# Kernel tuning notes

Measured on AMD Instinct MI355X. Metric: run time of the kernel, lower is better.

Reference implementation:

```python
import jax, jax.numpy as jnp
import numpy as np

FEA, DK, H = 512, 64, 8
B, L = 4, 2048
EPS = 1e-5


def _layernorm(x, g, b):
    mu = jnp.mean(x, axis=-1, keepdims=True)
    var = jnp.mean(jnp.square(x - mu), axis=-1, keepdims=True)
    return (x - mu) * jax.lax.rsqrt(var + EPS) * g + b


def setup_inputs() -> dict:
    key = jax.random.key(0)
    ks = jax.random.split(key, 12)
    d = {
        'qx': jax.random.normal(ks[0], (B, L, FEA), jnp.float32),
        'kx': jax.random.normal(ks[1], (B, L, FEA), jnp.float32),
        'vx': jax.random.normal(ks[2], (B, L, FEA), jnp.float32),
        'maskPAD': jax.random.randint(ks[3], (B, L, L), 0, 2, jnp.int32),
        # attention projections (stored as [in, out]); biases zero-init as in module
        'wq': jax.random.normal(ks[4], (FEA, DK * H), jnp.float32) * 0.02,
        'bq': jnp.zeros((DK * H,), jnp.float32),
        'wk': jax.random.normal(ks[5], (FEA, DK * H), jnp.float32) * 0.02,
        'bk': jnp.zeros((DK * H,), jnp.float32),
        'wv': jax.random.normal(ks[6], (FEA, DK * H), jnp.float32) * 0.02,
        'bv': jnp.zeros((DK * H,), jnp.float32),
        'wo': jax.random.normal(ks[7], (DK * H, FEA), jnp.float32) * 0.02,
        'bo': jnp.zeros((FEA,), jnp.float32),
        # FFN
        'w1': jax.random.normal(ks[8], (FEA, 4 * FEA), jnp.float32) * 0.02,
        'b1': jnp.zeros((4 * FEA,), jnp.float32),
        'w2': jax.random.normal(ks[9], (4 * FEA, FEA), jnp.float32) * 0.02,
        'b2': jnp.zeros((FEA,), jnp.float32),
        # layer norms
        'ln1_g': jnp.ones((FEA,), jnp.float32),
        'ln1_b': jnp.zeros((FEA,), jnp.float32),
        'ln2_g': jnp.ones((FEA,), jnp.float32),
        'ln2_b': jnp.zeros((FEA,), jnp.float32),
    }
    return d


def reference(qx, kx, vx, maskPAD, wq, bq, wk, bk, wv, bv, wo, bo,
              w1, b1, w2, b2, ln1_g, ln1_b, ln2_g, ln2_b):
    b, l, _ = qx.shape
    # project and split heads: [B, H, L, DK]
    q = (qx @ wq + bq).reshape(b, l, H, DK).transpose(0, 2, 1, 3)
    k = (kx @ wk + bk).reshape(b, l, H, DK).transpose(0, 2, 1, 3)
    v = (vx @ wv + bv).reshape(b, l, H, DK).transpose(0, 2, 1, 3)
    scores = jnp.einsum('bhqd,bhkd->bhqk', q, k) / np.sqrt(DK)  # [B,H,L,L]
    mask = (maskPAD == 0)[:, None, :, :]
    scores = jnp.where(mask, jnp.float32(-2 ** 15 + 1), scores)
    alpha = jax.nn.softmax(scores, axis=-1)
    z = jnp.einsum('bhqk,bhkd->bhqd', alpha, v)  # [B,H,L,DK]
    z = z.transpose(0, 2, 1, 3).reshape(b, l, H * DK)
    z = z @ wo + bo
    # post-LN FFN block (dropout = identity at inference)
    zn = _layernorm(vx + z, ln1_g, ln1_b)
    ffn = jax.nn.gelu(zn @ w1 + b1, approximate=False) @ w2 + b2
    return _layernorm(zn + ffn, ln2_g, ln2_b)
```

## Files before the change

### kernel.cpp

```cpp
#include <hip/hip_runtime.h>
#include <cstdint>


typedef __bf16 bf16;
typedef __bf16 bf16x8 __attribute__((ext_vector_type(8)));
typedef __bf16 bf16x4 __attribute__((ext_vector_type(4)));
typedef float floatx4 __attribute__((ext_vector_type(4)));

__device__ __forceinline__ floatx4 mfma_bf16(bf16x8 a, bf16x8 b, floatx4 c) {
  return __builtin_amdgcn_mfma_f32_16x16x32_bf16(a, b, c, 0, 0, 0);
}

__device__ __forceinline__ void load_lds_16(const void* g, void* l) {
  auto gp = reinterpret_cast<const void __attribute__((address_space(1)))*>(
      reinterpret_cast<uintptr_t>(g));
  auto lp = reinterpret_cast<void __attribute__((address_space(3)))*>(
      (unsigned int)reinterpret_cast<uintptr_t>(l));
  __builtin_amdgcn_global_load_lds(gp, lp, 16, 0, 0);
}

__device__ __forceinline__ float gelu_f(float x) {
  float t = 0.7978845608f * (x + 0.044715f * x * x * x);
  float e = __builtin_amdgcn_exp2f(t * 2.885390082f);
  float th = 1.0f - 2.0f * __builtin_amdgcn_rcpf(e + 1.0f);
  return 0.5f * x * (1.0f + th);
}

#define PLANE128 2064
#define PLANE64 1040
#define PSTR 72

__global__ void __launch_bounds__(256) transpose4_k(const float* __restrict__ w0,
                                                    const float* __restrict__ w1,
                                                    const float* __restrict__ w2,
                                                    const float* __restrict__ w3,
                                                    bf16* __restrict__ o0,
                                                    bf16* __restrict__ o1,
                                                    bf16* __restrict__ o2,
                                                    bf16* __restrict__ o3) {
  const float* in = (blockIdx.z == 0) ? w0 : (blockIdx.z == 1) ? w1
                    : (blockIdx.z == 2) ? w2 : w3;
  bf16* out = (blockIdx.z == 0) ? o0 : (blockIdx.z == 1) ? o1
              : (blockIdx.z == 2) ? o2 : o3;
  __shared__ float tile[32][33];
  int m0 = blockIdx.x * 32, k0 = blockIdx.y * 32;
  int tx = threadIdx.x, ty = threadIdx.y;
  for (int i = ty; i < 32; i += 8)
    tile[i][tx] = in[(size_t)(k0 + i) * 512 + m0 + tx];
  __syncthreads();
  for (int i = ty; i < 32; i += 8)
    out[(size_t)(m0 + i) * 512 + k0 + tx] = (bf16)tile[tx][i];
}

__global__ void __launch_bounds__(256) transpose_k(const float* __restrict__ in,
                                                   bf16* __restrict__ out,
                                                   int K, int M) {
  __shared__ float tile[32][33];
  int m0 = blockIdx.x * 32, k0 = blockIdx.y * 32;
  int tx = threadIdx.x, ty = threadIdx.y;
  for (int i = ty; i < 32; i += 8)
    tile[i][tx] = in[(size_t)(k0 + i) * M + m0 + tx];
  __syncthreads();
  for (int i = ty; i < 32; i += 8)
    out[(size_t)(m0 + i) * K + k0 + tx] = (bf16)tile[tx][i];
}

__global__ void __launch_bounds__(256) maskbits_k(const int* __restrict__ m,
                                                  unsigned long long* __restrict__ out) {
  int w = blockIdx.x * 4 + (threadIdx.x >> 6);
  int lane = threadIdx.x & 63;
  int v = m[(size_t)w * 64 + lane];
  unsigned long long b = __ballot(v != 0);
  if (lane == 0) out[w] = b;
}

template <int EPI>
__device__ __forceinline__ void epi_store(void* Cout, int n, int m, int M,
                                          float val) {
  if constexpr (EPI == 1) {
    int bb = n >> 11, l = n & 2047, hh = m >> 6, d = m & 63;
    ((bf16*)Cout)[((size_t)((bb * 8 + hh) * 2048 + l)) * 64 + d] = (bf16)val;
  } else if constexpr (EPI == 2) {
    int bb = n >> 11, l = n & 2047, hh = m >> 6, d = m & 63;
    ((bf16*)Cout)[((size_t)((bb * 8 + hh) * 64 + d)) * 2048 + l] = (bf16)val;
  } else if constexpr (EPI == 3) {
    ((bf16*)Cout)[(size_t)n * M + m] = (bf16)gelu_f(val);
  } else if constexpr (EPI == 4) {
    ((float*)Cout)[(size_t)n * M + m] = val;
  } else {
    ((float*)Cout)[(size_t)n * M + m] += val;
  }
}

template <int EPI, bool TALL>
__global__ void __launch_bounds__(256) gemm_bt(const bf16* __restrict__ A,
                                               const bf16* __restrict__ Bt,
                                               const float* __restrict__ bias,
                                               void* __restrict__ Cout,
                                               int M, int K, int lda, int ldb) {
  __shared__ __attribute__((aligned(16))) char As[8 * PLANE128];
  __shared__ __attribute__((aligned(16))) char Bs[TALL ? 8 * PLANE64 : 8 * PLANE128];
  int tid = threadIdx.x, wave = tid >> 6, lane = tid & 63;
  int lrow = lane & 15, quad = lane >> 4;
  int n0 = blockIdx.y * 128;
  int m0 = blockIdx.x * (TALL ? 64 : 128);
  int wr = wave >> 1, wc = wave & 1;
  floatx4 zero4 = {0.f, 0.f, 0.f, 0.f};
  constexpr int NI = TALL ? 2 : 4;
  floatx4 acc[NI][4];
#pragma unroll
  for (int i = 0; i < NI; ++i)
#pragma unroll
    for (int j = 0; j < 4; ++j) acc[i][j] = zero4;
  for (int k0 = 0; k0 < K; k0 += 64) {
    __syncthreads();
#pragma unroll
    for (int h = 0; h < 2; ++h) {
      int p = wave + 4 * h;
#pragma unroll
      for (int j = 0; j < 2; ++j) {
        int row = j * 64 + lane;
        load_lds_16(A + (size_t)(n0 + row) * lda + k0 + p * 8,
                    As + p * PLANE128 + j * 1024 + lane * 16);
      }
      if constexpr (TALL) {
        load_lds_16(Bt + (size_t)(m0 + lane) * ldb + k0 + p * 8,
                    Bs + p * PLANE64 + lane * 16);
      } else {
#pragma unroll
        for (int j = 0; j < 2; ++j) {
          int row = j * 64 + lane;
          load_lds_16(Bt + (size_t)(m0 + row) * ldb + k0 + p * 8,
                      Bs + p * PLANE128 + j * 1024 + lane * 16);
        }
      }
    }
    __syncthreads();
#pragma unroll
    for (int h = 0; h < 2; ++h) {
      int pb = h * 4 + quad;
      bf16x8 af[NI], bfr[4];
#pragma unroll
      for (int i = 0; i < NI; ++i) {
        int row = (TALL ? wave * 32 : wr * 64) + i * 16 + lrow;
        af[i] = *(const bf16x8*)(As + pb * PLANE128 + row * 16);
      }
#pragma unroll
      for (int j = 0; j < 4; ++j) {
        if constexpr (TALL)
          bfr[j] = *(const bf16x8*)(Bs + pb * PLANE64 + (j * 16 + lrow) * 16);
        else
          bfr[j] = *(const bf16x8*)(Bs + pb * PLANE128 +
                                    (wc * 64 + j * 16 + lrow) * 16);
      }
#pragma unroll
      for (int i = 0; i < NI; ++i)
#pragma unroll
        for (int j = 0; j < 4; ++j)
          acc[i][j] = mfma_bf16(af[i], bfr[j], acc[i][j]);
    }
  }
  float bv[4];
#pragma unroll
  for (int j = 0; j < 4; ++j) {
    int m = m0 + (TALL ? 0 : wc * 64) + j * 16 + lrow;
    bv[j] = (EPI == 5) ? 0.f : bias[m];
  }
#pragma unroll
  for (int i = 0; i < NI; ++i)
#pragma unroll
    for (int j = 0; j < 4; ++j)
#pragma unroll
      for (int r = 0; r < 4; ++r) {
        int n = n0 + (TALL ? wave * 32 : wr * 64) + i * 16 + quad * 4 + r;
        int m = m0 + (TALL ? 0 : wc * 64) + j * 16 + lrow;
        epi_store<EPI>(Cout, n, m, M, acc[i][j][r] + bv[j]);
      }
}

__global__ void __launch_bounds__(256) qkv_k(const float* __restrict__ qx,
                                             const float* __restrict__ kx,
                                             const float* __restrict__ vx,
                                             const bf16* __restrict__ wqT,
                                             const bf16* __restrict__ wkT,
                                             const bf16* __restrict__ wvT,
                                             const float* __restrict__ bq,
                                             const float* __restrict__ bk,
                                             const float* __restrict__ bv_,
                                             bf16* __restrict__ qh,
                                             bf16* __restrict__ kh,
                                             bf16* __restrict__ vt) {
  __shared__ __attribute__((aligned(16))) char As[8 * PLANE128];
  __shared__ __attribute__((aligned(16))) char Bs[8 * PLANE128];
  int tid = threadIdx.x, wave = tid >> 6, lane = tid & 63;
  int lrow = lane & 15, quad = lane >> 4;
  int seg = blockIdx.y >> 6;
  int n0 = (blockIdx.y & 63) * 128, m0 = blockIdx.x * 128;
  const float* Af = (seg == 0) ? qx : (seg == 1) ? kx : vx;
  const bf16* Bt = (seg == 0) ? wqT : (seg == 1) ? wkT : wvT;
  const float* bias = (seg == 0) ? bq : (seg == 1) ? bk : bv_;
  bf16* out = (seg == 0) ? qh : (seg == 1) ? kh : vt;
  int wr = wave >> 1, wc = wave & 1;
  floatx4 zero4 = {0.f, 0.f, 0.f, 0.f};
  floatx4 acc[4][4];
#pragma unroll
  for (int i = 0; i < 4; ++i)
#pragma unroll
    for (int j = 0; j < 4; ++j) acc[i][j] = zero4;
  int arow = tid >> 2, ap = tid & 3;
  for (int k0 = 0; k0 < 512; k0 += 64) {
    bf16x8 a[4];
#pragma unroll
    for (int u = 0; u < 4; ++u) {
      int row = arow + (u & 1) * 64, p = ap + (u >> 1) * 4;
      const float* src = Af + (size_t)(n0 + row) * 512 + k0 + p * 8;
      float4 x0 = *(const float4*)src;
      float4 x1 = *(const float4*)(src + 4);
      a[u][0] = (bf16)x0.x; a[u][1] = (bf16)x0.y; a[u][2] = (bf16)x0.z;
      a[u][3] = (bf16)x0.w; a[u][4] = (bf16)x1.x; a[u][5] = (bf16)x1.y;
      a[u][6] = (bf16)x1.z; a[u][7] = (bf16)x1.w;
    }
    __syncthreads();
#pragma unroll
    for (int u = 0; u < 4; ++u) {
      int row = arow + (u & 1) * 64, p = ap + (u >> 1) * 4;
      *(bf16x8*)(As + p * PLANE128 + row * 16) = a[u];
    }
#pragma unroll
    for (int h = 0; h < 2; ++h) {
      int p = wave + 4 * h;
#pragma unroll
      for (int j = 0; j < 2; ++j) {
        int row = j * 64 + lane;
        load_lds_16(Bt + (size_t)(m0 + row) * 512 + k0 + p * 8,
                    Bs + p * PLANE128 + j * 1024 + lane * 16);
      }
    }
    __syncthreads();
#pragma unroll
    for (int h = 0; h < 2; ++h) {
      int pb = h * 4 + quad;
      bf16x8 af[4], bfr[4];
#pragma unroll
      for (int t = 0; t < 4; ++t) {
        af[t] = *(const bf16x8*)(As + pb * PLANE128 + (wr * 64 + t * 16 + lrow) * 16);
        bfr[t] = *(const bf16x8*)(Bs + pb * PLANE128 + (wc * 64 + t * 16 + lrow) * 16);
      }
#pragma unroll
      for (int i = 0; i < 4; ++i)
#pragma unroll
        for (int j = 0; j < 4; ++j) acc[i][j] = mfma_bf16(af[i], bfr[j], acc[i][j]);
    }
  }
  float bvv[4];
#pragma unroll
  for (int j = 0; j < 4; ++j) bvv[j] = bias[m0 + wc * 64 + j * 16 + lrow];
#pragma unroll
  for (int i = 0; i < 4; ++i)
#pragma unroll
    for (int j = 0; j < 4; ++j)
#pragma unroll
      for (int r = 0; r < 4; ++r) {
        int n = n0 + wr * 64 + i * 16 + quad * 4 + r;
        int m = m0 + wc * 64 + j * 16 + lrow;
        float val = acc[i][j][r] + bvv[j];
        int bb = n >> 11, l = n & 2047, hh = m >> 6, d = m & 63;
        if (seg == 2)
          out[((size_t)((bb * 8 + hh) * 64 + d)) * 2048 + l] = (bf16)val;
        else
          out[((size_t)((bb * 8 + hh) * 2048 + l)) * 64 + d] = (bf16)val;
      }
}

__global__ void __launch_bounds__(256) attn_k(const bf16* __restrict__ Qh,
                                              const bf16* __restrict__ Kh,
                                              const bf16* __restrict__ Vt,
                                              const unsigned long long* __restrict__ MB,
                                              bf16* __restrict__ Z) {
  __shared__ __attribute__((aligned(16))) char Ks[8 * PLANE64];
  __shared__ __attribute__((aligned(16))) char Vs[8 * PLANE64];
  __shared__ __attribute__((aligned(16))) bf16 Ps[4][16 * PSTR];
  int qt = blockIdx.x, h = blockIdx.y, b = blockIdx.z;
  int tid = threadIdx.x, wave = tid >> 6, lane = tid & 63;
  int lrow = lane & 15, quad = lane >> 4;
  int q0 = qt * 64;
  size_t headbase = (size_t)(b * 8 + h) * 2048 * 64;

  const bf16* Qp = Qh + headbase + (size_t)(q0 + wave * 16 + lrow) * 64 + quad * 8;
  bf16x8 qf0 = *(const bf16x8*)Qp;
  bf16x8 qf1 = *(const bf16x8*)(Qp + 32);

  floatx4 zero4 = {0.f, 0.f, 0.f, 0.f};
  floatx4 o_acc[4], acc_l = zero4;
#pragma unroll
  for (int dt = 0; dt < 4; ++dt) o_acc[dt] = zero4;
  bf16x8 ones;
#pragma unroll
  for (int j = 0; j < 8; ++j) ones[j] = (bf16)1.0f;

  const bf16* Vg = Vt + headbase;
  const uint2* MBb =
      (const uint2*)(MB + ((size_t)b * 2048 + q0 + wave * 16 + lrow) * 32);
  bf16* Pw = Ps[wave];
  const float C = 0.1803368801f;
  int sh = quad * 4;

  for (int kt = 0; kt < 32; ++kt) {
    int kk0 = kt * 64;
    const bf16* Kg = Kh + headbase + (size_t)kk0 * 64;
    __syncthreads();
#pragma unroll
    for (int j = 0; j < 2; ++j) {
      int p = wave * 2 + j;
      load_lds_16(Kg + (size_t)lane * 64 + p * 8, Ks + p * PLANE64 + lane * 16);
      load_lds_16(Vg + (size_t)lane * 2048 + kk0 + p * 8,
                  Vs + p * PLANE64 + lane * 16);
    }
    uint2 mw = MBb[kt];
    __syncthreads();

#pragma unroll
    for (int nt = 0; nt < 4; ++nt) {
      int R = nt * 16 + lrow;
      bf16x8 k0f = *(const bf16x8*)(Ks + quad * PLANE64 + R * 16);
      bf16x8 k1f = *(const bf16x8*)(Ks + (quad + 4) * PLANE64 + R * 16);
      floatx4 aa = zero4;
      aa = mfma_bf16(k0f, qf0, aa);
      aa = mfma_bf16(k1f, qf1, aa);
      floatx4 sc = aa * C;
      unsigned wn = ((nt & 2) ? mw.y : mw.x) >> ((nt & 1) * 16 + sh);
      bf16x4 pv;
#pragma unroll
      for (int r = 0; r < 4; ++r) {
        float e = __builtin_amdgcn_exp2f(sc[r]);
        pv[r] = (bf16)((wn & (1u << r)) ? e : 0.f);
      }
      *(bf16x4*)(Pw + lrow * PSTR + nt * 16 + quad * 4) = pv;
    }
    bf16x8 pf0 = *(const bf16x8*)(Pw + lrow * PSTR + quad * 8);
    bf16x8 pf1 = *(const bf16x8*)(Pw + lrow * PSTR + 32 + quad * 8);
    acc_l = mfma_bf16(pf0, ones, acc_l);
    acc_l = mfma_bf16(pf1, ones, acc_l);
#pragma unroll
    for (int dt = 0; dt < 4; ++dt) {
      int R = dt * 16 + lrow;
      bf16x8 v0 = *(const bf16x8*)(Vs + quad * PLANE64 + R * 16);
      bf16x8 v1 = *(const bf16x8*)(Vs + (quad + 4) * PLANE64 + R * 16);
      o_acc[dt] = mfma_bf16(pf0, v0, o_acc[dt]);
      o_acc[dt] = mfma_bf16(pf1, v1, o_acc[dt]);
    }
  }
  float lr[4];
#pragma unroll
  for (int r = 0; r < 4; ++r) lr[r] = 1.0f / acc_l[r];
#pragma unroll
  for (int dt = 0; dt < 4; ++dt)
#pragma unroll
    for (int r = 0; r < 4; ++r) {
      int qrow = q0 + wave * 16 + quad * 4 + r;
      int d = dt * 16 + lrow;
      Z[((size_t)(b * 2048 + qrow)) * 512 + h * 64 + d] = (bf16)(o_acc[dt][r] * lr[r]);
    }
}

template <bool A_BF16, bool OUT_BF16>
__global__ void __launch_bounds__(256) ln_k(const void* __restrict__ a_,
                                            const float* __restrict__ s,
                                            const float* __restrict__ g,
                                            const float* __restrict__ bta,
                                            void* __restrict__ out_) {
  int row = blockIdx.x * 4 + (threadIdx.x >> 6);
  int lane = threadIdx.x & 63;
  size_t base = (size_t)row * 512 + lane * 8;
  float x[8];
  float4 sa = *(const float4*)(s + base);
  float4 sb = *(const float4*)(s + base + 4);
  if constexpr (A_BF16) {
    bf16x8 av = *(const bf16x8*)((const bf16*)a_ + base);
    x[0] = (float)av[0] + sa.x; x[1] = (float)av[1] + sa.y;
    x[2] = (float)av[2] + sa.z; x[3] = (float)av[3] + sa.w;
    x[4] = (float)av[4] + sb.x; x[5] = (float)av[5] + sb.y;
    x[6] = (float)av[6] + sb.z; x[7] = (float)av[7] + sb.w;
  } else {
    float4 a0 = *(const float4*)((const float*)a_ + base);
    float4 a1 = *(const float4*)((const float*)a_ + base + 4);
    x[0] = a0.x + sa.x; x[1] = a0.y + sa.y; x[2] = a0.z + sa.z; x[3] = a0.w + sa.w;
    x[4] = a1.x + sb.x; x[5] = a1.y + sb.y; x[6] = a1.z + sb.z; x[7] = a1.w + sb.w;
  }
  float sum = 0.f;
#pragma unroll
  for (int i = 0; i < 8; ++i) sum += x[i];
#pragma unroll
  for (int off = 1; off < 64; off <<= 1) sum += __shfl_xor(sum, off, 64);
  float mu = sum * (1.0f / 512.0f);
  float vs = 0.f;
#pragma unroll
  for (int i = 0; i < 8; ++i) { float d = x[i] - mu; vs += d * d; }
#pragma unroll
  for (int off = 1; off < 64; off <<= 1) vs += __shfl_xor(vs, off, 64);
  float rstd = rsqrtf(vs * (1.0f / 512.0f) + 1e-5f);
  float4 g0 = *(const float4*)(g + lane * 8);
  float4 g1 = *(const float4*)(g + lane * 8 + 4);
  float4 b0 = *(const float4*)(bta + lane * 8);
  float4 b1 = *(const float4*)(bta + lane * 8 + 4);
  float gg[8] = {g0.x, g0.y, g0.z, g0.w, g1.x, g1.y, g1.z, g1.w};
  float bb[8] = {b0.x, b0.y, b0.z, b0.w, b1.x, b1.y, b1.z, b1.w};
  if constexpr (OUT_BF16) {
    bf16x8 o;
#pragma unroll
    for (int i = 0; i < 8; ++i)
      o[i] = (bf16)((x[i] - mu) * rstd * gg[i] + bb[i]);
    *(bf16x8*)((bf16*)out_ + base) = o;
  } else {
    float4 o0, o1;
    o0.x = (x[0] - mu) * rstd * gg[0] + bb[0];
    o0.y = (x[1] - mu) * rstd * gg[1] + bb[1];
    o0.z = (x[2] - mu) * rstd * gg[2] + bb[2];
    o0.w = (x[3] - mu) * rstd * gg[3] + bb[3];
    o1.x = (x[4] - mu) * rstd * gg[4] + bb[4];
    o1.y = (x[5] - mu) * rstd * gg[5] + bb[5];
    o1.z = (x[6] - mu) * rstd * gg[6] + bb[6];
    o1.w = (x[7] - mu) * rstd * gg[7] + bb[7];
    *(float4*)((float*)out_ + base) = o0;
    *(float4*)((float*)out_ + base + 4) = o1;
  }
}

extern "C" void kernel_launch(void* const* d_in, const int* in_sizes, int n_in,
                              void* d_out, int out_size, void* d_ws, size_t ws_size,
                              hipStream_t stream) {
  const float* qx = (const float*)d_in[0];
  const float* kx = (const float*)d_in[1];
  const float* vx = (const float*)d_in[2];
  const int* maskPAD = (const int*)d_in[3];
  const float* wq = (const float*)d_in[4];
  const float* bq = (const float*)d_in[5];
  const float* wk = (const float*)d_in[6];
  const float* bk = (const float*)d_in[7];
  const float* wv = (const float*)d_in[8];
  const float* bv = (const float*)d_in[9];
  const float* wo = (const float*)d_in[10];
  const float* bo = (const float*)d_in[11];
  const float* w1 = (const float*)d_in[12];
  const float* b1 = (const float*)d_in[13];
  const float* w2 = (const float*)d_in[14];
  const float* b2 = (const float*)d_in[15];
  const float* g1 = (const float*)d_in[16];
  const float* be1 = (const float*)d_in[17];
  const float* g2 = (const float*)d_in[18];
  const float* be2 = (const float*)d_in[19];

  char* w = (char*)d_ws;
  size_t off = 0;
  auto alloc = [&](size_t bytes) {
    void* p = w + off;
    off += (bytes + 255) & ~(size_t)255;
    return p;
  };
  bf16* wqT = (bf16*)alloc(512 * 512 * 2);
  bf16* wkT = (bf16*)alloc(512 * 512 * 2);
  bf16* wvT = (bf16*)alloc(512 * 512 * 2);
  bf16* woT = (bf16*)alloc(512 * 512 * 2);
  bf16* w1T = (bf16*)alloc(2048 * 512 * 2);
  bf16* w2T = (bf16*)alloc(512 * 2048 * 2);
  unsigned long long* mbits = (unsigned long long*)alloc((size_t)4 * 2048 * 32 * 8);
  bf16* qh = (bf16*)alloc((size_t)8192 * 512 * 2);
  bf16* kh = (bf16*)alloc((size_t)8192 * 512 * 2);
  bf16* vt = (bf16*)alloc((size_t)8192 * 512 * 2);
  bf16* z = (bf16*)alloc((size_t)8192 * 512 * 2);
  float* s12 = (float*)qh;
  bf16* zn = vt;
  size_t h1_bytes = (size_t)8192 * 2048 * 2;
  bool big = (off + h1_bytes) <= ws_size;
  bf16* h1 = big ? (bf16*)alloc(h1_bytes) : z;

  dim3 tb(32, 8);
  transpose4_k<<<dim3(16, 16, 4), tb, 0, stream>>>(wq, wk, wv, wo, wqT, wkT, wvT, woT);
  transpose_k<<<dim3(64, 16), tb, 0, stream>>>(w1, w1T, 512, 2048);
  transpose_k<<<dim3(16, 64), tb, 0, stream>>>(w2, w2T, 2048, 512);
  maskbits_k<<<65536, 256, 0, stream>>>(maskPAD, mbits);
  qkv_k<<<dim3(4, 192), 256, 0, stream>>>(qx, kx, vx, wqT, wkT, wvT, bq, bk, bv,
                                          qh, kh, vt);
  attn_k<<<dim3(32, 8, 4), 256, 0, stream>>>(qh, kh, vt, mbits, z);
  gemm_bt<4, true><<<dim3(8, 64), 256, 0, stream>>>(z, woT, bo, s12, 512, 512,
                                                    512, 512);
  ln_k<false, true><<<2048, 256, 0, stream>>>(vx, s12, g1, be1, zn);
  if (big) {
    gemm_bt<3, false><<<dim3(16, 64), 256, 0, stream>>>(zn, w1T, b1, h1, 2048,
                                                        512, 512, 512);
    gemm_bt<4, true><<<dim3(8, 64), 256, 0, stream>>>(h1, w2T, b2, s12, 512,
                                                      2048, 2048, 2048);
  } else {
    for (int p = 0; p < 4; ++p) {
      gemm_bt<3, true><<<dim3(8, 64), 256, 0, stream>>>(
          zn, w1T + (size_t)p * 512 * 512, b1 + p * 512, h1, 512, 512, 512, 512);
      if (p == 0)
        gemm_bt<4, true><<<dim3(8, 64), 256, 0, stream>>>(
            h1, w2T + p * 512, b2, s12, 512, 512, 512, 2048);
      else
        gemm_bt<5, true><<<dim3(8, 64), 256, 0, stream>>>(
            h1, w2T + p * 512, nullptr, s12, 512, 512, 512, 2048);
    }
  }
  ln_k<true, false><<<2048, 256, 0, stream>>>(zn, s12, g2, be2, (float*)d_out);
}
```

Before: 459.6 us.

## Double-buffer K/V tiles and process two query subtiles per wave in attention

The attention kernel now loads the next K/V tile into a second LDS buffer while computing on the current one, which removes one barrier per iteration. Each wave handles 32 query rows instead of 16, so each K/V fragment read from LDS feeds twice as many MFMAs, and the grid is halved to match. In exchange the kernel uses more LDS and registers, which may lower occupancy, and launches only 512 blocks, which may underfill the GPU.

Measured after the change: 436.2 us. -5.1%, faster.

```diff
diff --git a/kernel.cpp b/kernel.cpp
--- a/kernel.cpp
+++ b/kernel.cpp
@@ -277,90 +277,128 @@
                                               const bf16* __restrict__ Vt,
                                               const unsigned long long* __restrict__ MB,
                                               bf16* __restrict__ Z) {
-  __shared__ __attribute__((aligned(16))) char Ks[8 * PLANE64];
-  __shared__ __attribute__((aligned(16))) char Vs[8 * PLANE64];
-  __shared__ __attribute__((aligned(16))) bf16 Ps[4][16 * PSTR];
+  __shared__ __attribute__((aligned(16))) char Ks[2][8 * PLANE64];
+  __shared__ __attribute__((aligned(16))) char Vs[2][8 * PLANE64];
+  __shared__ __attribute__((aligned(16))) bf16 Ps[4][32 * PSTR];
   int qt = blockIdx.x, h = blockIdx.y, b = blockIdx.z;
   int tid = threadIdx.x, wave = tid >> 6, lane = tid & 63;
   int lrow = lane & 15, quad = lane >> 4;
-  int q0 = qt * 64;
+  int q0 = qt * 128;
   size_t headbase = (size_t)(b * 8 + h) * 2048 * 64;
 
-  const bf16* Qp = Qh + headbase + (size_t)(q0 + wave * 16 + lrow) * 64 + quad * 8;
-  bf16x8 qf0 = *(const bf16x8*)Qp;
-  bf16x8 qf1 = *(const bf16x8*)(Qp + 32);
+  bf16x8 qf[2][2];
+#pragma unroll
+  for (int u = 0; u < 2; ++u) {
+    const bf16* Qp =
+        Qh + headbase + (size_t)(q0 + wave * 32 + u * 16 + lrow) * 64 + quad * 8;
+    qf[u][0] = *(const bf16x8*)Qp;
+    qf[u][1] = *(const bf16x8*)(Qp + 32);
+  }
 
   floatx4 zero4 = {0.f, 0.f, 0.f, 0.f};
-  floatx4 o_acc[4], acc_l = zero4;
-#pragma unroll
-  for (int dt = 0; dt < 4; ++dt) o_acc[dt] = zero4;
+  floatx4 o_acc[2][4], acc_l[2];
+#pragma unroll
+  for (int u = 0; u < 2; ++u) {
+    acc_l[u] = zero4;
+#pragma unroll
+    for (int dt = 0; dt < 4; ++dt) o_acc[u][dt] = zero4;
+  }
   bf16x8 ones;
 #pragma unroll
   for (int j = 0; j < 8; ++j) ones[j] = (bf16)1.0f;
 
   const bf16* Vg = Vt + headbase;
-  const uint2* MBb =
-      (const uint2*)(MB + ((size_t)b * 2048 + q0 + wave * 16 + lrow) * 32);
+  const bf16* Kg0 = Kh + headbase;
+  const uint2* MB0 =
+      (const uint2*)(MB + ((size_t)b * 2048 + q0 + wave * 32 + lrow) * 32);
   bf16* Pw = Ps[wave];
   const float C = 0.1803368801f;
   int sh = quad * 4;
 
-  for (int kt = 0; kt < 32; ++kt) {
-    int kk0 = kt * 64;
-    const bf16* Kg = Kh + headbase + (size_t)kk0 * 64;
-    __syncthreads();
+  auto stage = [&](int buf, int kt) {
+    int kk = kt * 64;
+    const bf16* Kg = Kg0 + (size_t)kk * 64;
 #pragma unroll
     for (int j = 0; j < 2; ++j) {
       int p = wave * 2 + j;
-      load_lds_16(Kg + (size_t)lane * 64 + p * 8, Ks + p * PLANE64 + lane * 16);
-      load_lds_16(Vg + (size_t)lane * 2048 + kk0 + p * 8,
-                  Vs + p * PLANE64 + lane * 16);
-    }
-    uint2 mw = MBb[kt];
+      load_lds_16(Kg + (size_t)lane * 64 + p * 8,
+                  Ks[buf] + p * PLANE64 + lane * 16);
+      load_lds_16(Vg + (size_t)lane * 2048 + kk + p * 8,
+                  Vs[buf] + p * PLANE64 + lane * 16);
+    }
+  };
+
+  stage(0, 0);
+  uint2 mwc[2] = {MB0[0], MB0[512]};
+
+  for (int kt = 0; kt < 32; ++kt) {
+    int cur = kt & 1;
     __syncthreads();
-
+    uint2 mwn[2];
+    if (kt < 31) {
+      stage(cur ^ 1, kt + 1);
+      mwn[0] = MB0[kt + 1];
+      mwn[1] = MB0[512 + kt + 1];
+    }
+    const char* Kc = Ks[cur];
+    const char* Vc = Vs[cur];
 #pragma unroll
     for (int nt = 0; nt < 4; ++nt) {
       int R = nt * 16 + lrow;
-      bf16x8 k0f = *(const bf16x8*)(Ks + quad * PLANE64 + R * 16);
-      bf16x8 k1f = *(const bf16x8*)(Ks + (quad + 4) * PLANE64 + R * 16);
-      floatx4 aa = zero4;
-      aa = mfma_bf16(k0f, qf0, aa);
-      aa = mfma_bf16(k1f, qf1, aa);
-      floatx4 sc = aa * C;
-      unsigned wn = ((nt & 2) ? mw.y : mw.x) >> ((nt & 1) * 16 + sh);
-      bf16x4 pv;
-#pragma unroll
-      for (int r = 0; r < 4; ++r) {
-        float e = __builtin_amdgcn_exp2f(sc[r]);
-        pv[r] = (bf16)((wn & (1u << r)) ? e : 0.f);
-      }
-      *(bf16x4*)(Pw + lrow * PSTR + nt * 16 + quad * 4) = pv;
-    }
-    bf16x8 pf0 = *(const bf16x8*)(Pw + lrow * PSTR + quad * 8);
-    bf16x8 pf1 = *(const bf16x8*)(Pw + lrow * PSTR + 32 + quad * 8);
-    acc_l = mfma_bf16(pf0, ones, acc_l);
-    acc_l = mfma_bf16(pf1, ones, acc_l);
+      bf16x8 k0f = *(const bf16x8*)(Kc + quad * PLANE64 + R * 16);
+      bf16x8 k1f = *(const bf16x8*)(Kc + (quad + 4) * PLANE64 + R * 16);
+#pragma unroll
+      for (int u = 0; u < 2; ++u) {
+        floatx4 aa = zero4;
+        aa = mfma_bf16(k0f, qf[u][0], aa);
+        aa = mfma_bf16(k1f, qf[u][1], aa);
+        floatx4 sc = aa * C;
+        unsigned wn = ((nt & 2) ? mwc[u].y : mwc[u].x) >> ((nt & 1) * 16 + sh);
+        bf16x4 pv;
+#pragma unroll
+        for (int r = 0; r < 4; ++r) {
+          float e = __builtin_amdgcn_exp2f(sc[r]);
+          pv[r] = (bf16)((wn & (1u << r)) ? e : 0.f);
+        }
+        *(bf16x4*)(Pw + (u * 16 + lrow) * PSTR + nt * 16 + quad * 4) = pv;
+      }
+    }
+    bf16x8 v0[4], v1[4];
 #pragma unroll
     for (int dt = 0; dt < 4; ++dt) {
       int R = dt * 16 + lrow;
-      bf16x8 v0 = *(const bf16x8*)(Vs + quad * PLANE64 + R * 16);
-      bf16x8 v1 = *(const bf16x8*)(Vs + (quad + 4) * PLANE64 + R * 16);
-      o_acc[dt] = mfma_bf16(pf0, v0, o_acc[dt]);
-      o_acc[dt] = mfma_bf16(pf1, v1, o_acc[dt]);
-    }
-  }
-  float lr[4];
-#pragma unroll
-  for (int r = 0; r < 4; ++r) lr[r] = 1.0f / acc_l[r];
-#pragma unroll
-  for (int dt = 0; dt < 4; ++dt)
-#pragma unroll
-    for (int r = 0; r < 4; ++r) {
-      int qrow = q0 + wave * 16 + quad * 4 + r;
-      int d = dt * 16 + lrow;
-      Z[((size_t)(b * 2048 + qrow)) * 512 + h * 64 + d] = (bf16)(o_acc[dt][r] * lr[r]);
-    }
+      v0[dt] = *(const bf16x8*)(Vc + quad * PLANE64 + R * 16);
+      v1[dt] = *(const bf16x8*)(Vc + (quad + 4) * PLANE64 + R * 16);
+    }
+#pragma unroll
+    for (int u = 0; u < 2; ++u) {
+      bf16x8 pf0 = *(const bf16x8*)(Pw + (u * 16 + lrow) * PSTR + quad * 8);
+      bf16x8 pf1 = *(const bf16x8*)(Pw + (u * 16 + lrow) * PSTR + 32 + quad * 8);
+      acc_l[u] = mfma_bf16(pf0, ones, acc_l[u]);
+      acc_l[u] = mfma_bf16(pf1, ones, acc_l[u]);
+#pragma unroll
+      for (int dt = 0; dt < 4; ++dt) {
+        o_acc[u][dt] = mfma_bf16(pf0, v0[dt], o_acc[u][dt]);
+        o_acc[u][dt] = mfma_bf16(pf1, v1[dt], o_acc[u][dt]);
+      }
+    }
+    if (kt < 31) { mwc[0] = mwn[0]; mwc[1] = mwn[1]; }
+  }
+#pragma unroll
+  for (int u = 0; u < 2; ++u) {
+    float lr[4];
+#pragma unroll
+    for (int r = 0; r < 4; ++r) lr[r] = 1.0f / acc_l[u][r];
+#pragma unroll
+    for (int dt = 0; dt < 4; ++dt)
+#pragma unroll
+      for (int r = 0; r < 4; ++r) {
+        int qrow = q0 + wave * 32 + u * 16 + quad * 4 + r;
+        int d = dt * 16 + lrow;
+        Z[((size_t)(b * 2048 + qrow)) * 512 + h * 64 + d] =
+            (bf16)(o_acc[u][dt][r] * lr[r]);
+      }
+  }
 }
 
 template <bool A_BF16, bool OUT_BF16>
@@ -481,7 +519,7 @@
   maskbits_k<<<65536, 256, 0, stream>>>(maskPAD, mbits);
   qkv_k<<<dim3(4, 192), 256, 0, stream>>>(qx, kx, vx, wqT, wkT, wvT, bq, bk, bv,
                                           qh, kh, vt);
-  attn_k<<<dim3(32, 8, 4), 256, 0, stream>>>(qh, kh, vt, mbits, z);
+  attn_k<<<dim3(16, 8, 4), 256, 0, stream>>>(qh, kh, vt, mbits, z);
   gemm_bt<4, true><<<dim3(8, 64), 256, 0, stream>>>(z, woT, bo, s12, 512, 512,
                                                     512, 512);
   ln_k<false, true><<<2048, 256, 0, stream>>>(vx, s12, g1, be1, zn);
```
